# Performance work log

Measured on AMD Instinct MI355X. Metric: run time of the kernel, lower is better.

The kernel has to match this reference:

```python
import jax, jax.numpy as jnp
from jax import lax
import numpy as np

B, H, W, D_MODEL = 2, 64, 64, 192
D_INNER, D_STATE, DT_RANK = 384, 16, 12
L = H * W
LN_EPS = 1e-5


def setup_inputs() -> dict:
    ks = jax.random.split(jax.random.key(0), 12)
    rng = np.random.default_rng(0)
    perm = rng.permutation(L).astype(np.int32)

    def p(i, shape, scale=0.02):
        return jax.random.normal(ks[i], shape, dtype=jnp.float32) * scale

    return {
        "x": jax.random.normal(ks[0], (B, H, W, D_MODEL), dtype=jnp.float32),
        "condition": jax.random.normal(ks[1], (B, H, W, D_MODEL), dtype=jnp.float32),
        "W_in": p(2, (2 * D_INNER, D_MODEL)),
        "W_con": p(3, (D_INNER, D_MODEL)),
        "conv_w": p(4, (D_INNER, 1, 3, 3)),
        "conv_b": jnp.zeros((D_INNER,), jnp.float32),
        "con_conv_w": p(5, (D_INNER, 1, 3, 3)),
        "con_conv_b": jnp.zeros((D_INNER,), jnp.float32),
        "x_proj_w": p(6, (DT_RANK + 2 * D_STATE, D_INNER)),
        "dt_proj_w": p(7, (D_INNER, DT_RANK)),
        "dt_proj_b": p(8, (D_INNER,), 0.1),
        "A_logs": jnp.tile(jnp.log(jnp.arange(1, D_STATE + 1, dtype=jnp.float32))[None, :], (D_INNER, 1)),
        "Ds": jnp.ones((D_INNER,), jnp.float32),
        "ln_w": jnp.ones((D_INNER,), jnp.float32),
        "ln_b": jnp.zeros((D_INNER,), jnp.float32),
        "W_out": p(9, (D_MODEL, D_INNER)),
        "scan_path": jnp.asarray(perm),
        "rev_scan_path": jnp.asarray(np.argsort(perm).astype(np.int32)),
    }


def _dwconv(x, w, b):
    # depthwise 3x3 conv, SAME padding; x: [B, C, H, W], w: [C, 1, 3, 3]
    y = lax.conv_general_dilated(x, w, (1, 1), "SAME",
                                 dimension_numbers=("NCHW", "OIHW", "NCHW"),
                                 feature_group_count=x.shape[1])
    return y + b[None, :, None, None]


def _selective_scan(u, delta, A, Bs, Cs, D):
    # u, delta: [B, D, L]; A: [D, N]; Bs, Cs: [B, N, L]; D: [D]
    dA = jnp.exp(jnp.einsum("bdl,dn->lbdn", delta, A))          # [L, B, D, N]
    dBu = jnp.einsum("bdl,bnl,bdl->lbdn", delta, Bs, u)          # [L, B, D, N]
    Ct = jnp.transpose(Cs, (2, 0, 1))                             # [L, B, N]
    h0 = jnp.zeros(dA.shape[1:], dA.dtype)

    def step(h, inp):
        a, b, c = inp
        h = a * h + b
        return h, jnp.einsum("bdn,bn->bd", h, c)

    _, ys = lax.scan(step, h0, (dA, dBu, Ct))                     # ys: [L, B, D]
    y = jnp.transpose(ys, (1, 2, 0))                              # [B, D, L]
    return y + u * D[None, :, None]


def _forward(x, condition, W_in, W_con, conv_w, conv_b, con_conv_w, con_conv_b,
             x_proj_w, dt_proj_w, dt_proj_b, A_logs, Ds, ln_w, ln_b, W_out,
             scan_path, rev_scan_path):
    b, h, w, _ = x.shape
    l = h * w
    xz = x @ W_in.T                                               # [B, H, W, 2*Din]
    xa, z = jnp.split(xz, 2, axis=-1)
    z = jax.nn.silu(z)
    c = condition @ W_con.T
    xa = jax.nn.silu(_dwconv(jnp.transpose(xa, (0, 3, 1, 2)), conv_w, conv_b))
    c = jax.nn.silu(_dwconv(jnp.transpose(c, (0, 3, 1, 2)), con_conv_w, con_conv_b))
    d = xa.shape[1]
    xs = xa.reshape(b, d, l)[:, :, scan_path]                     # forward_permutation, K=1
    cs = c.reshape(b, d, l)[:, :, scan_path]
    x_dbl = jnp.einsum("bdl,cd->bcl", xs + cs, x_proj_w)          # [B, R+2N, L]
    r, n = dt_proj_w.shape[1], A_logs.shape[1]
    dts = jnp.einsum("brl,dr->bdl", x_dbl[:, :r], dt_proj_w)
    Bs = x_dbl[:, r:r + n]
    Cs = x_dbl[:, r + n:]
    A = -jnp.exp(A_logs)
    delta = jax.nn.softplus(dts + dt_proj_b[None, :, None])       # delta_softplus=True
    y = _selective_scan(xs, delta, A, Bs, Cs, Ds)                 # [B, D, L]
    y = y[:, :, rev_scan_path]                                    # backward_permutation
    y = jnp.transpose(y, (0, 2, 1))                               # [B, L, D]
    mu = jnp.mean(y, axis=-1, keepdims=True)
    var = jnp.var(y, axis=-1, keepdims=True)
    y = (y - mu) * lax.rsqrt(var + LN_EPS) * ln_w + ln_b          # out_norm
    y = y.reshape(b, h, w, d) * z
    return y @ W_out.T                                            # out_proj (no bias)


def reference(x, condition, W_in, W_con, conv_w, conv_b, con_conv_w, con_conv_b,
              x_proj_w, dt_proj_w, dt_proj_b, A_logs, Ds, ln_w, ln_b, W_out,
              scan_path, rev_scan_path):
    return _forward(x, condition, W_in, W_con, conv_w, conv_b, con_conv_w,
                    con_conv_b, x_proj_w, dt_proj_w, dt_proj_b, A_logs, Ds,
                    ln_w, ln_b, W_out, scan_path, rev_scan_path)
```

## Files before the change

### kernel.cpp

```cpp
#include <hip/hip_runtime.h>
#include <math.h>

#define BB 2
#define HH 64
#define WW 64
#define DM 192
#define DI 384
#define NS 16
#define DTR 12
#define LL 4096
#define ROWS (BB*LL)
#define NCHUNK 128
#define LCHUNK 32
#define NCOMBP 512
#define CSTRIDE ((size_t)BB * DI * 8)

typedef __attribute__((ext_vector_type(8))) short bf16x8;
typedef __attribute__((ext_vector_type(4))) float f32x4;

typedef __attribute__((address_space(3))) void        as3_void;
typedef __attribute__((address_space(1))) const void  as1_cvoid;

__device__ __forceinline__ void gl_lds16(const unsigned short* g, unsigned short* l) {
    __builtin_amdgcn_global_load_lds((as1_cvoid*)g, (as3_void*)l, 16, 0, 0);
}

__device__ __forceinline__ float silu_f(float v) {
    return v / (1.0f + __expf(-v));
}

__device__ __forceinline__ unsigned short f2bf(float f) {
    union { float f; unsigned int u; } c; c.f = f;
    unsigned int u = c.u;
    u += 0x7fffu + ((u >> 16) & 1u);
    return (unsigned short)(u >> 16);
}
__device__ __forceinline__ float bf2f(unsigned short h) {
    union { unsigned int u; float f; } c; c.u = ((unsigned int)h) << 16;
    return c.f;
}

__global__ __launch_bounds__(256) void prep_weights(
    const float* __restrict__ x, const float* __restrict__ cond,
    const float* __restrict__ w_in, const float* __restrict__ w_con,
    const float* __restrict__ w_out,
    const float* __restrict__ x_proj_w, const float* __restrict__ dt_w,
    unsigned short* __restrict__ w_in_bf, unsigned short* __restrict__ w_con_bf,
    unsigned short* __restrict__ w_out_bf, unsigned short* __restrict__ wc,
    unsigned short* __restrict__ x_bfo, unsigned short* __restrict__ c_bfo)
{
    int idx = blockIdx.x * 256 + threadIdx.x;
    if (idx < 73728) {
        const float4* src; ushort4* dst; int off;
        if (idx < 36864)      { src = (const float4*)w_in;  dst = (ushort4*)w_in_bf;  off = idx; }
        else if (idx < 55296) { src = (const float4*)w_con; dst = (ushort4*)w_con_bf; off = idx - 36864; }
        else                  { src = (const float4*)w_out; dst = (ushort4*)w_out_bf; off = idx - 55296; }
        float4 v = src[off];
        ushort4 o;
        o.x = f2bf(v.x); o.y = f2bf(v.y); o.z = f2bf(v.z); o.w = f2bf(v.w);
        dst[off] = o;
    } else if (idx < 73728 + NCOMBP * DI) {
        int e = idx - 73728;
        int row = e / DI, k = e - row * DI;
        float v = 0.f;
        if (row < 384) {
            const float* dw = dt_w + row * DTR;
            #pragma unroll
            for (int r = 0; r < DTR; ++r) v += dw[r] * x_proj_w[r * DI + k];
        } else if (row < 416) {
            v = x_proj_w[(12 + (row - 384)) * DI + k];
        }
        wc[e] = f2bf(v);
    } else if (idx < 73728 + NCOMBP * DI + 786432) {
        int e = idx - (73728 + NCOMBP * DI);
        const float4* src; ushort4* dst; int off;
        if (e < 393216) { src = (const float4*)x;    dst = (ushort4*)x_bfo; off = e; }
        else            { src = (const float4*)cond; dst = (ushort4*)c_bfo; off = e - 393216; }
        float4 v = src[off];
        ushort4 o;
        o.x = f2bf(v.x); o.y = f2bf(v.y); o.z = f2bf(v.z); o.w = f2bf(v.w);
        dst[off] = o;
    }
}

__global__ __launch_bounds__(256) void gemm_in(
    const unsigned short* __restrict__ x_bf, const unsigned short* __restrict__ cin_bf,
    const unsigned short* __restrict__ w_in_bf,
    const unsigned short* __restrict__ w_con_bf,
    unsigned short* __restrict__ xa_bf, unsigned short* __restrict__ z_bf,
    unsigned short* __restrict__ c_bf)
{
    const int zz = blockIdx.z;
    if (zz == 1 && blockIdx.y >= 3) return;
    const unsigned short* A = zz ? cin_bf : x_bf;
    const unsigned short* W = zz ? w_con_bf : w_in_bf;

    __shared__ __align__(16) unsigned short sA[128 * 32];
    __shared__ __align__(16) unsigned short sB[128 * 32];
    const int bm = blockIdx.x * 128;
    const int bn = blockIdx.y * 128;
    const int tid  = threadIdx.x;
    const int wave = tid >> 6;
    const int lane = tid & 63;
    const int quad = lane >> 4;
    const int l16  = lane & 15;
    const int srow = tid >> 2;
    const int scol = (tid & 3) * 8;

    f32x4 acc[2][8];
    #pragma unroll
    for (int rf = 0; rf < 2; ++rf)
        #pragma unroll
        for (int t = 0; t < 8; ++t) acc[rf][t] = (f32x4)(0.f);

    const unsigned short* gA0 = &A[(size_t)(bm + srow) * DM + scol];
    const unsigned short* gA1 = gA0 + (size_t)64 * DM;
    const unsigned short* gB0 = &W[(size_t)(bn + srow) * DM + scol];
    const unsigned short* gB1 = gB0 + (size_t)64 * DM;
    unsigned short* lA0 = &sA[wave * 512];
    unsigned short* lA1 = &sA[2048 + wave * 512];
    unsigned short* lB0 = &sB[wave * 512];
    unsigned short* lB1 = &sB[2048 + wave * 512];

    const int ar0 = (wave * 32 + l16) * 32 + quad * 8;
    const int ar1 = ar0 + 16 * 32;

    for (int k0 = 0; k0 < DM; k0 += 32) {
        gl_lds16(gA0 + k0, lA0);
        gl_lds16(gA1 + k0, lA1);
        gl_lds16(gB0 + k0, lB0);
        gl_lds16(gB1 + k0, lB1);
        __syncthreads();
        bf16x8 a0 = *(bf16x8*)&sA[ar0];
        bf16x8 a1 = *(bf16x8*)&sA[ar1];
        #pragma unroll
        for (int t = 0; t < 8; ++t) {
            bf16x8 b = *(bf16x8*)&sB[(t * 16 + l16) * 32 + quad * 8];
            acc[0][t] = __builtin_amdgcn_mfma_f32_16x16x32_bf16(a0, b, acc[0][t], 0, 0, 0);
            acc[1][t] = __builtin_amdgcn_mfma_f32_16x16x32_bf16(a1, b, acc[1][t], 0, 0, 0);
        }
        __syncthreads();
    }

    #pragma unroll
    for (int rf = 0; rf < 2; ++rf) {
        #pragma unroll
        for (int t = 0; t < 8; ++t) {
            int col = bn + t * 16 + l16;
            #pragma unroll
            for (int r = 0; r < 4; ++r) {
                int row = bm + wave * 32 + rf * 16 + quad * 4 + r;
                float v = acc[rf][t][r];
                if (zz == 0) {
                    if (col < 384) xa_bf[(size_t)row * 384 + col] = f2bf(v);
                    else           z_bf[(size_t)row * 384 + (col - 384)] = f2bf(silu_f(v));
                } else {
                    c_bf[(size_t)row * 384 + col] = f2bf(v);
                }
            }
        }
    }
}

__global__ __launch_bounds__(256) void gemm_comb(
    const unsigned short* __restrict__ A, const unsigned short* __restrict__ W,
    const float* __restrict__ bias, float* __restrict__ btct,
    unsigned short* __restrict__ du_lo)
{
    __shared__ __align__(16) unsigned short sA[128 * 32];
    __shared__ __align__(16) unsigned short sB[128 * 32];
    const int bm = blockIdx.x * 128;
    const int bn = blockIdx.y * 128;
    const int tid  = threadIdx.x;
    const int wave = tid >> 6;
    const int lane = tid & 63;
    const int quad = lane >> 4;
    const int l16  = lane & 15;
    const int srow = tid >> 2;
    const int scol = (tid & 3) * 8;

    f32x4 acc[2][8];
    #pragma unroll
    for (int rf = 0; rf < 2; ++rf)
        #pragma unroll
        for (int t = 0; t < 8; ++t) acc[rf][t] = (f32x4)(0.f);

    const unsigned short* gA0 = &A[(size_t)(bm + srow) * DI + scol];
    const unsigned short* gA1 = gA0 + (size_t)64 * DI;
    const unsigned short* gB0 = &W[(size_t)(bn + srow) * DI + scol];
    const unsigned short* gB1 = gB0 + (size_t)64 * DI;
    unsigned short* lA0 = &sA[wave * 512];
    unsigned short* lA1 = &sA[2048 + wave * 512];
    unsigned short* lB0 = &sB[wave * 512];
    unsigned short* lB1 = &sB[2048 + wave * 512];

    const int ar0 = (wave * 32 + l16) * 32 + quad * 8;
    const int ar1 = ar0 + 16 * 32;

    for (int k0 = 0; k0 < DI; k0 += 32) {
        gl_lds16(gA0 + k0, lA0);
        gl_lds16(gA1 + k0, lA1);
        gl_lds16(gB0 + k0, lB0);
        gl_lds16(gB1 + k0, lB1);
        __syncthreads();
        bf16x8 a0 = *(bf16x8*)&sA[ar0];
        bf16x8 a1 = *(bf16x8*)&sA[ar1];
        #pragma unroll
        for (int t = 0; t < 8; ++t) {
            bf16x8 b = *(bf16x8*)&sB[(t * 16 + l16) * 32 + quad * 8];
            acc[0][t] = __builtin_amdgcn_mfma_f32_16x16x32_bf16(a0, b, acc[0][t], 0, 0, 0);
            acc[1][t] = __builtin_amdgcn_mfma_f32_16x16x32_bf16(a1, b, acc[1][t], 0, 0, 0);
        }
        __syncthreads();
    }

    #pragma unroll
    for (int rf = 0; rf < 2; ++rf) {
        #pragma unroll
        for (int t = 0; t < 8; ++t) {
            int col = bn + t * 16 + l16;
            #pragma unroll
            for (int r = 0; r < 4; ++r) {
                int row = bm + wave * 32 + rf * 16 + quad * 4 + r;
                float v = acc[rf][t][r];
                if (col < 384) {
                    float a = v + bias[col];
                    float sp = (a > 20.f) ? a : log1pf(__expf(a));
                    du_lo[((size_t)row * 384 + col) * 2] = f2bf(sp);
                } else if (col < 416) {
                    int idx = col - 384;
                    int pos = (idx < 16) ? ((idx & 7) * 4 + (idx >> 3))
                                         : (((idx - 16) & 7) * 4 + 2 + ((idx - 16) >> 3));
                    btct[(size_t)row * 32 + pos] = v;
                }
            }
        }
    }
}

__global__ __launch_bounds__(256) void gemm_out_fused(
    const unsigned short* __restrict__ yt, const unsigned short* __restrict__ z,
    const int* __restrict__ rev_path,
    const float* __restrict__ ln_w, const float* __restrict__ ln_b,
    const unsigned short* __restrict__ W, float* __restrict__ out)
{
    __shared__ __align__(16) unsigned short sA[64 * 392];
    __shared__ __align__(16) unsigned short sB[64 * 32];
    const int bm = blockIdx.x * 64;
    const int bn = blockIdx.y * 64;
    const int tid = threadIdx.x;
    const int r   = tid >> 2;
    const int q4  = tid & 3;
    const int b   = bm >> 12;
    const int l   = (bm & (LL - 1)) + r;
    const int js  = rev_path[l];

    const unsigned short* yrow = yt + ((size_t)(b * LL + js)) * DI;
    const unsigned short* zrow = z  + ((size_t)(b * LL + l)) * DI;

    float s = 0.f, s2 = 0.f;
    #pragma unroll
    for (int i = 0; i < 12; ++i) {
        bf16x8 v = *(const bf16x8*)&yrow[i * 32 + q4 * 8];
        #pragma unroll
        for (int e = 0; e < 8; ++e) {
            float f = bf2f((unsigned short)v[e]);
            s += f; s2 += f * f;
        }
    }
    s  += __shfl_xor(s, 1);  s  += __shfl_xor(s, 2);
    s2 += __shfl_xor(s2, 1); s2 += __shfl_xor(s2, 2);
    const float mu  = s * (1.0f / DI);
    const float inv = rsqrtf(s2 * (1.0f / DI) - mu * mu + 1e-5f);

    #pragma unroll
    for (int i = 0; i < 12; ++i) {
        int c = i * 32 + q4 * 8;
        bf16x8 v  = *(const bf16x8*)&yrow[c];
        bf16x8 zv = *(const bf16x8*)&zrow[c];
        float4 wa = *(const float4*)&ln_w[c];
        float4 wb = *(const float4*)&ln_w[c + 4];
        float4 ba = *(const float4*)&ln_b[c];
        float4 bb = *(const float4*)&ln_b[c + 4];
        bf16x8 o;
        o[0] = (short)f2bf(((bf2f((unsigned short)v[0]) - mu) * inv * wa.x + ba.x) * bf2f((unsigned short)zv[0]));
        o[1] = (short)f2bf(((bf2f((unsigned short)v[1]) - mu) * inv * wa.y + ba.y) * bf2f((unsigned short)zv[1]));
        o[2] = (short)f2bf(((bf2f((unsigned short)v[2]) - mu) * inv * wa.z + ba.z) * bf2f((unsigned short)zv[2]));
        o[3] = (short)f2bf(((bf2f((unsigned short)v[3]) - mu) * inv * wa.w + ba.w) * bf2f((unsigned short)zv[3]));
        o[4] = (short)f2bf(((bf2f((unsigned short)v[4]) - mu) * inv * wb.x + bb.x) * bf2f((unsigned short)zv[4]));
        o[5] = (short)f2bf(((bf2f((unsigned short)v[5]) - mu) * inv * wb.y + bb.y) * bf2f((unsigned short)zv[5]));
        o[6] = (short)f2bf(((bf2f((unsigned short)v[6]) - mu) * inv * wb.z + bb.z) * bf2f((unsigned short)zv[6]));
        o[7] = (short)f2bf(((bf2f((unsigned short)v[7]) - mu) * inv * wb.w + bb.w) * bf2f((unsigned short)zv[7]));
        *(bf16x8*)&sA[r * 392 + c] = o;
    }

    const int wave = tid >> 6;
    const int lane = tid & 63;
    const int quad = lane >> 4;
    const int l16  = lane & 15;

    f32x4 acc[4];
    #pragma unroll
    for (int t = 0; t < 4; ++t) acc[t] = (f32x4)(0.f);

    const unsigned short* gB = &W[(size_t)(bn + r) * DI + q4 * 8];
    unsigned short* lB = &sB[wave * 512];
    const int abase = (wave * 16 + l16) * 392 + quad * 8;

    for (int k0 = 0; k0 < DI; k0 += 32) {
        gl_lds16(gB + k0, lB);
        __syncthreads();
        bf16x8 a = *(bf16x8*)&sA[abase + k0];
        #pragma unroll
        for (int t = 0; t < 4; ++t) {
            bf16x8 bfr = *(bf16x8*)&sB[(t * 16 + l16) * 32 + quad * 8];
            acc[t] = __builtin_amdgcn_mfma_f32_16x16x32_bf16(a, bfr, acc[t], 0, 0, 0);
        }
        __syncthreads();
    }

    #pragma unroll
    for (int t = 0; t < 4; ++t) {
        int col = bn + t * 16 + l16;
        #pragma unroll
        for (int rr = 0; rr < 4; ++rr) {
            int row = bm + wave * 16 + quad * 4 + rr;
            out[(size_t)row * DM + col] = acc[t][rr];
        }
    }
}

__global__ __launch_bounds__(256) void dwconv2_scatter(
    const unsigned short* __restrict__ xin, const unsigned short* __restrict__ cin,
    const float* __restrict__ wx, const float* __restrict__ bx,
    const float* __restrict__ wc, const float* __restrict__ bc,
    const int* __restrict__ rev_scan_path,
    unsigned short* __restrict__ du_hi,
    unsigned short* __restrict__ s_bf)
{
    const int tile = blockIdx.x;
    const int c0   = blockIdx.y * 32;
    const int b    = blockIdx.z;
    const int h0 = (tile >> 3) * 8, w0 = (tile & 7) * 8;
    __shared__ float smx[10 * 10 * 32];
    __shared__ float smc[10 * 10 * 32];
    __shared__ int   jtile[64];

    for (int idx = threadIdx.x; idx < 3200; idx += 256) {
        int pix = idx >> 5, ch = idx & 31;
        int py = pix / 10, px = pix - py * 10;
        int gh = h0 + py - 1, gw = w0 + px - 1;
        float vx = 0.f, vc = 0.f;
        if (gh >= 0 && gh < 64 && gw >= 0 && gw < 64) {
            size_t g = ((size_t)(b * LL + gh * 64 + gw)) * DI + c0 + ch;
            vx = bf2f(xin[g]); vc = bf2f(cin[g]);
        }
        smx[idx] = vx; smc[idx] = vc;
    }
    if (threadIdx.x < 64) {
        int l = (h0 + (threadIdx.x >> 3)) * 64 + (w0 + (threadIdx.x & 7));
        jtile[threadIdx.x] = rev_scan_path[l];
    }
    __syncthreads();

    const int ch = threadIdx.x & 31;
    const int pq = threadIdx.x >> 5;
    float wrx[9], wrc[9];
    #pragma unroll
    for (int k = 0; k < 9; ++k) {
        wrx[k] = wx[(c0 + ch) * 9 + k];
        wrc[k] = wc[(c0 + ch) * 9 + k];
    }
    const float bvx = bx[c0 + ch];
    const float bvc = bc[c0 + ch];

    #pragma unroll
    for (int i = 0; i < 8; ++i) {
        int p  = pq * 8 + i;
        int ph = p >> 3, pw = p & 7;
        float ax = bvx, ac = bvc;
        #pragma unroll
        for (int ki = 0; ki < 3; ++ki)
            #pragma unroll
            for (int kj = 0; kj < 3; ++kj) {
                int si = ((ph + ki) * 10 + (pw + kj)) * 32 + ch;
                ax += wrx[ki * 3 + kj] * smx[si];
                ac += wrc[ki * 3 + kj] * smc[si];
            }
        float xv = silu_f(ax);
        float sv = xv + silu_f(ac);
        size_t o = ((size_t)(b * LL + jtile[p])) * DI + c0 + ch;
        du_hi[o * 2 + 1] = f2bf(xv);
        s_bf[o]          = f2bf(sv);
    }
}

__global__ __launch_bounds__(256) void scan_chunkA(
    const unsigned int* __restrict__ du, const float* __restrict__ btct,
    const float* __restrict__ A_logs,
    float* __restrict__ chunkA, float* __restrict__ chunkB)
{
    const int c = blockIdx.x;
    const int g = blockIdx.y;
    const int b = blockIdx.z;
    const int t = threadIdx.x;
    const int grp = t >> 3, p = t & 7;
    const int d = g * 32 + grp;
    const float Av0 = -__expf(A_logs[d * NS + p]);
    const float Av1 = -__expf(A_logs[d * NS + p + 8]);
    const int j0 = c * LCHUNK;

    const unsigned int* dul = du + ((size_t)b * LL + j0) * DI + d;
    const float2*       bl  = (const float2*)btct + ((size_t)b * LL + j0) * 16 + p * 2;

    float h0 = 0.f, h1 = 0.f, Sd = 0.f;
    unsigned int duv[4]; float2 bv[4];
    #pragma unroll
    for (int q = 0; q < 4; ++q) {
        duv[q] = dul[(size_t)q * DI]; bv[q] = bl[(size_t)q * 16];
    }
    for (int j = 0; j < LCHUNK; j += 4) {
        unsigned int ndu[4]; float2 nb[4];
        if (j + 4 < LCHUNK) {
            #pragma unroll
            for (int q = 0; q < 4; ++q) {
                int jj = j + 4 + q;
                ndu[q] = dul[(size_t)jj * DI]; nb[q] = bl[(size_t)jj * 16];
            }
        }
        #pragma unroll
        for (int q = 0; q < 4; ++q) {
            float dv = bf2f((unsigned short)(duv[q] & 0xffff));
            float uv = bf2f((unsigned short)(duv[q] >> 16));
            float e0 = __expf(dv * Av0);
            float e1 = __expf(dv * Av1);
            float duu = dv * uv;
            h0 = e0 * h0 + bv[q].x * duu;
            h1 = e1 * h1 + bv[q].y * duu;
            Sd += dv;
        }
        #pragma unroll
        for (int q = 0; q < 4; ++q) { duv[q]=ndu[q]; bv[q]=nb[q]; }
    }
    size_t idx = (size_t)c * CSTRIDE + ((size_t)b * DI + d) * 8 + p;
    ((float2*)chunkA)[idx] = make_float2(__expf(Sd * Av0), __expf(Sd * Av1));
    ((float2*)chunkB)[idx] = make_float2(h0, h1);
}

__global__ __launch_bounds__(256) void scan_chunkC(
    const unsigned int* __restrict__ du, const float* __restrict__ btct,
    const float* __restrict__ A_logs, const float* __restrict__ Ds,
    const float* __restrict__ chunkA, const float* __restrict__ chunkB,
    unsigned short* __restrict__ yt)
{
    const int c = blockIdx.x;
    const int g = blockIdx.y;
    const int b = blockIdx.z;
    const int t = threadIdx.x;
    const int grp = t >> 3, p = t & 7;
    const int d = g * 32 + grp;
    const float Av0 = -__expf(A_logs[d * NS + p]);
    const float Av1 = -__expf(A_logs[d * NS + p + 8]);
    const float Dv = Ds[d];
    const int j0 = c * LCHUNK;

    const unsigned int* dul = du + ((size_t)b * LL + j0) * DI + d;
    const float4*       bcl = (const float4*)btct + ((size_t)b * LL + j0) * 8 + p;
    unsigned short* yl = yt + ((size_t)b * LL + j0) * DI + d;

    const size_t off = ((size_t)b * DI + d) * 8 + p;
    const float2* A2 = (const float2*)chunkA;
    const float2* B2 = (const float2*)chunkB;
    float h0 = 0.f, h1 = 0.f, P0 = 1.f, P1 = 1.f;
    for (int i = c - 1; i >= 0; --i) {
        size_t ix = (size_t)i * CSTRIDE + off;
        float2 a = A2[ix], bv = B2[ix];
        h0 += P0 * bv.x;  h1 += P1 * bv.y;
        P0 *= a.x;        P1 *= a.y;
        if (fmaxf(fabsf(P0), fabsf(P1)) < 1e-30f) break;
    }

    unsigned int duv[4]; float4 bc[4];
    #pragma unroll
    for (int q = 0; q < 4; ++q) {
        duv[q] = dul[(size_t)q * DI]; bc[q] = bcl[(size_t)q * 8];
    }
    for (int j = 0; j < LCHUNK; j += 4) {
        unsigned int ndu[4]; float4 nbc[4];
        if (j + 4 < LCHUNK) {
            #pragma unroll
            for (int q = 0; q < 4; ++q) {
                int jj = j + 4 + q;
                ndu[q] = dul[(size_t)jj * DI]; nbc[q] = bcl[(size_t)jj * 8];
            }
        }
        #pragma unroll
        for (int q = 0; q < 4; ++q) {
            float dv = bf2f((unsigned short)(duv[q] & 0xffff));
            float uv = bf2f((unsigned short)(duv[q] >> 16));
            float e0 = __expf(dv * Av0);
            float e1 = __expf(dv * Av1);
            float duu = dv * uv;
            h0 = e0 * h0 + bc[q].x * duu;
            h1 = e1 * h1 + bc[q].y * duu;
            float acc = h0 * bc[q].z + h1 * bc[q].w;
            acc += __shfl_xor(acc, 4, 8);
            acc += __shfl_xor(acc, 2, 8);
            acc += __shfl_xor(acc, 1, 8);
            if (p == 0) yl[(size_t)(j + q) * DI] = f2bf(acc + uv * Dv);
        }
        #pragma unroll
        for (int q = 0; q < 4; ++q) { duv[q]=ndu[q]; bc[q]=nbc[q]; }
    }
}

extern "C" void kernel_launch(void* const* d_in, const int* in_sizes, int n_in,
                              void* d_out, int out_size, void* d_ws, size_t ws_size,
                              hipStream_t stream) {
    const float* x          = (const float*)d_in[0];
    const float* cond       = (const float*)d_in[1];
    const float* W_in       = (const float*)d_in[2];
    const float* W_con      = (const float*)d_in[3];
    const float* conv_w     = (const float*)d_in[4];
    const float* conv_b     = (const float*)d_in[5];
    const float* con_conv_w = (const float*)d_in[6];
    const float* con_conv_b = (const float*)d_in[7];
    const float* x_proj_w   = (const float*)d_in[8];
    const float* dt_proj_w  = (const float*)d_in[9];
    const float* dt_proj_b  = (const float*)d_in[10];
    const float* A_logs     = (const float*)d_in[11];
    const float* Ds         = (const float*)d_in[12];
    const float* ln_w       = (const float*)d_in[13];
    const float* ln_b       = (const float*)d_in[14];
    const float* W_out      = (const float*)d_in[15];
    const int*   scan_path  = (const int*)d_in[16];
    const int*   rev_path   = (const int*)d_in[17];
    (void)scan_path;

    float* ws = (float*)d_ws;
    const size_t S  = (size_t)BB * LL * DI;
    const size_t SC = (size_t)NCHUNK * BB * DI * NS;
    float* ytslab  = ws + 0 * S;
    float* zslab   = ws + 1 * S;
    float* duslab  = ws + 2 * S;
    float* btct    = ws + 3 * S;
    float* chunkA  = btct + (size_t)BB * LL * 32;
    float* chunkB  = chunkA + SC;
    float* bfpool  = chunkB + SC;

    unsigned short* yt_bf    = (unsigned short*)ytslab;
    unsigned short* z_bf     = (unsigned short*)zslab;
    unsigned int*   du       = (unsigned int*)duslab;
    unsigned short* s_bf     = (unsigned short*)bfpool;
    unsigned short* xa_bf    = s_bf + (size_t)ROWS * DI;
    unsigned short* c_bf     = xa_bf + (size_t)ROWS * DI;
    unsigned short* w_in_bf  = c_bf + (size_t)ROWS * DI;
    unsigned short* w_con_bf = w_in_bf + 768 * DM;
    unsigned short* w_out_bf = w_con_bf + 384 * DM;
    unsigned short* wcomb_bf = w_out_bf + 192 * DI;
    unsigned short* x_bf2    = wcomb_bf + (size_t)NCOMBP * DI;
    unsigned short* cin_bf2  = x_bf2 + (size_t)ROWS * DM;

    prep_weights<<<4128, 256, 0, stream>>>(
        x, cond, W_in, W_con, W_out, x_proj_w, dt_proj_w,
        w_in_bf, w_con_bf, w_out_bf, wcomb_bf, x_bf2, cin_bf2);

    gemm_in<<<dim3(ROWS / 128, 6, 2), 256, 0, stream>>>(
        x_bf2, cin_bf2, w_in_bf, w_con_bf, xa_bf, z_bf, c_bf);
    dwconv2_scatter<<<dim3(64, 12, BB), 256, 0, stream>>>(
        xa_bf, c_bf, conv_w, conv_b, con_conv_w, con_conv_b,
        rev_path, (unsigned short*)du, s_bf);
    gemm_comb<<<dim3(ROWS / 128, NCOMBP / 128), 256, 0, stream>>>(
        s_bf, wcomb_bf, dt_proj_b, btct, (unsigned short*)du);
    scan_chunkA<<<dim3(NCHUNK, DI / 32, BB), 256, 0, stream>>>(
        du, btct, A_logs, chunkA, chunkB);
    scan_chunkC<<<dim3(NCHUNK, DI / 32, BB), 256, 0, stream>>>(
        du, btct, A_logs, Ds, chunkA, chunkB, yt_bf);
    gemm_out_fused<<<dim3(ROWS / 64, DM / 64), 256, 0, stream>>>(
        yt_bf, z_bf, rev_path, ln_w, ln_b, w_out_bf, (float*)d_out);
}
```

Baseline: 227.4 us.

## Double-buffer and swizzle LDS in GEMMs, shrink N tile, trim padded comb rows

All three bf16 MFMA GEMMs now double-buffer their LDS tiles, so the next K-slice's global-to-LDS load is issued while the current slice is multiplied, and one barrier per iteration is removed. The LDS layout gets an XOR swizzle on the 16-byte column groups to cut bank conflicts on fragment reads. gemm_in and gemm_comb use a 64-wide N tile instead of 128, which doubles the block count for occupancy. The padded combined-weight matrix shrinks from 512 to 448 rows, removing wasted MFMA work. The costs are more LDS per block, fewer accumulators per wave (less reuse of each A fragment), and more blocks re-reading A.

```diff
diff --git a/kernel.cpp b/kernel.cpp
--- a/kernel.cpp
+++ b/kernel.cpp
@@ -12,7 +12,7 @@
 #define ROWS (BB*LL)
 #define NCHUNK 128
 #define LCHUNK 32
-#define NCOMBP 512
+#define NCOMB 448
 #define CSTRIDE ((size_t)BB * DI * 8)
 
 typedef __attribute__((ext_vector_type(8))) short bf16x8;
@@ -59,7 +59,7 @@
         ushort4 o;
         o.x = f2bf(v.x); o.y = f2bf(v.y); o.z = f2bf(v.z); o.w = f2bf(v.w);
         dst[off] = o;
-    } else if (idx < 73728 + NCOMBP * DI) {
+    } else if (idx < 73728 + NCOMB * DI) {
         int e = idx - 73728;
         int row = e / DI, k = e - row * DI;
         float v = 0.f;
@@ -71,8 +71,8 @@
             v = x_proj_w[(12 + (row - 384)) * DI + k];
         }
         wc[e] = f2bf(v);
-    } else if (idx < 73728 + NCOMBP * DI + 786432) {
-        int e = idx - (73728 + NCOMBP * DI);
+    } else if (idx < 73728 + NCOMB * DI + 786432) {
+        int e = idx - (73728 + NCOMB * DI);
         const float4* src; ushort4* dst; int off;
         if (e < 393216) { src = (const float4*)x;    dst = (ushort4*)x_bfo; off = e; }
         else            { src = (const float4*)cond; dst = (ushort4*)c_bfo; off = e - 393216; }
@@ -91,61 +91,67 @@
     unsigned short* __restrict__ c_bf)
 {
     const int zz = blockIdx.z;
-    if (zz == 1 && blockIdx.y >= 3) return;
+    if (zz == 1 && blockIdx.y >= 6) return;
     const unsigned short* A = zz ? cin_bf : x_bf;
     const unsigned short* W = zz ? w_con_bf : w_in_bf;
 
-    __shared__ __align__(16) unsigned short sA[128 * 32];
-    __shared__ __align__(16) unsigned short sB[128 * 32];
+    __shared__ __align__(16) unsigned short sA[2 * 128 * 32];
+    __shared__ __align__(16) unsigned short sB[2 * 64 * 32];
     const int bm = blockIdx.x * 128;
-    const int bn = blockIdx.y * 128;
+    const int bn = blockIdx.y * 64;
     const int tid  = threadIdx.x;
     const int wave = tid >> 6;
     const int lane = tid & 63;
     const int quad = lane >> 4;
     const int l16  = lane & 15;
     const int srow = tid >> 2;
-    const int scol = (tid & 3) * 8;
-
-    f32x4 acc[2][8];
+    const int scol = ((tid & 3) ^ ((tid >> 3) & 3)) * 8;
+    const int rswz = (quad ^ ((l16 >> 1) & 3)) * 8;
+
+    f32x4 acc[2][4];
     #pragma unroll
     for (int rf = 0; rf < 2; ++rf)
         #pragma unroll
-        for (int t = 0; t < 8; ++t) acc[rf][t] = (f32x4)(0.f);
+        for (int t = 0; t < 4; ++t) acc[rf][t] = (f32x4)(0.f);
 
     const unsigned short* gA0 = &A[(size_t)(bm + srow) * DM + scol];
     const unsigned short* gA1 = gA0 + (size_t)64 * DM;
-    const unsigned short* gB0 = &W[(size_t)(bn + srow) * DM + scol];
-    const unsigned short* gB1 = gB0 + (size_t)64 * DM;
-    unsigned short* lA0 = &sA[wave * 512];
-    unsigned short* lA1 = &sA[2048 + wave * 512];
-    unsigned short* lB0 = &sB[wave * 512];
-    unsigned short* lB1 = &sB[2048 + wave * 512];
-
-    const int ar0 = (wave * 32 + l16) * 32 + quad * 8;
+    const unsigned short* gB  = &W[(size_t)(bn + srow) * DM + scol];
+
+    gl_lds16(gA0, &sA[wave * 512]);
+    gl_lds16(gA1, &sA[2048 + wave * 512]);
+    gl_lds16(gB,  &sB[wave * 512]);
+    __syncthreads();
+
+    const int ar0 = (wave * 32 + l16) * 32 + rswz;
     const int ar1 = ar0 + 16 * 32;
 
-    for (int k0 = 0; k0 < DM; k0 += 32) {
-        gl_lds16(gA0 + k0, lA0);
-        gl_lds16(gA1 + k0, lA1);
-        gl_lds16(gB0 + k0, lB0);
-        gl_lds16(gB1 + k0, lB1);
+    for (int t = 0; t < 6; ++t) {
+        const int cur = t & 1;
+        if (t + 1 < 6) {
+            const int k = (t + 1) * 32;
+            const int nb = cur ^ 1;
+            gl_lds16(gA0 + k, &sA[nb * 4096 + wave * 512]);
+            gl_lds16(gA1 + k, &sA[nb * 4096 + 2048 + wave * 512]);
+            gl_lds16(gB  + k, &sB[nb * 2048 + wave * 512]);
+        }
+        const unsigned short* cA = &sA[cur * 4096];
+        const unsigned short* cB = &sB[cur * 2048];
+        bf16x8 a0 = *(bf16x8*)&cA[ar0];
+        bf16x8 a1 = *(bf16x8*)&cA[ar1];
+        #pragma unroll
+        for (int n = 0; n < 4; ++n) {
+            bf16x8 b = *(bf16x8*)&cB[(n * 16 + l16) * 32 + rswz];
+            acc[0][n] = __builtin_amdgcn_mfma_f32_16x16x32_bf16(a0, b, acc[0][n], 0, 0, 0);
+            acc[1][n] = __builtin_amdgcn_mfma_f32_16x16x32_bf16(a1, b, acc[1][n], 0, 0, 0);
+        }
         __syncthreads();
-        bf16x8 a0 = *(bf16x8*)&sA[ar0];
-        bf16x8 a1 = *(bf16x8*)&sA[ar1];
-        #pragma unroll
-        for (int t = 0; t < 8; ++t) {
-            bf16x8 b = *(bf16x8*)&sB[(t * 16 + l16) * 32 + quad * 8];
-            acc[0][t] = __builtin_amdgcn_mfma_f32_16x16x32_bf16(a0, b, acc[0][t], 0, 0, 0);
-            acc[1][t] = __builtin_amdgcn_mfma_f32_16x16x32_bf16(a1, b, acc[1][t], 0, 0, 0);
-        }
-        __syncthreads();
     }
 
     #pragma unroll
     for (int rf = 0; rf < 2; ++rf) {
         #pragma unroll
-        for (int t = 0; t < 8; ++t) {
+        for (int t = 0; t < 4; ++t) {
             int col = bn + t * 16 + l16;
             #pragma unroll
             for (int r = 0; r < 4; ++r) {
@@ -167,57 +173,63 @@
     const float* __restrict__ bias, float* __restrict__ btct,
     unsigned short* __restrict__ du_lo)
 {
-    __shared__ __align__(16) unsigned short sA[128 * 32];
-    __shared__ __align__(16) unsigned short sB[128 * 32];
+    __shared__ __align__(16) unsigned short sA[2 * 128 * 32];
+    __shared__ __align__(16) unsigned short sB[2 * 64 * 32];
     const int bm = blockIdx.x * 128;
-    const int bn = blockIdx.y * 128;
+    const int bn = blockIdx.y * 64;
     const int tid  = threadIdx.x;
     const int wave = tid >> 6;
     const int lane = tid & 63;
     const int quad = lane >> 4;
     const int l16  = lane & 15;
     const int srow = tid >> 2;
-    const int scol = (tid & 3) * 8;
-
-    f32x4 acc[2][8];
+    const int scol = ((tid & 3) ^ ((tid >> 3) & 3)) * 8;
+    const int rswz = (quad ^ ((l16 >> 1) & 3)) * 8;
+
+    f32x4 acc[2][4];
     #pragma unroll
     for (int rf = 0; rf < 2; ++rf)
         #pragma unroll
-        for (int t = 0; t < 8; ++t) acc[rf][t] = (f32x4)(0.f);
+        for (int t = 0; t < 4; ++t) acc[rf][t] = (f32x4)(0.f);
 
     const unsigned short* gA0 = &A[(size_t)(bm + srow) * DI + scol];
     const unsigned short* gA1 = gA0 + (size_t)64 * DI;
-    const unsigned short* gB0 = &W[(size_t)(bn + srow) * DI + scol];
-    const unsigned short* gB1 = gB0 + (size_t)64 * DI;
-    unsigned short* lA0 = &sA[wave * 512];
-    unsigned short* lA1 = &sA[2048 + wave * 512];
-    unsigned short* lB0 = &sB[wave * 512];
-    unsigned short* lB1 = &sB[2048 + wave * 512];
-
-    const int ar0 = (wave * 32 + l16) * 32 + quad * 8;
+    const unsigned short* gB  = &W[(size_t)(bn + srow) * DI + scol];
+
+    gl_lds16(gA0, &sA[wave * 512]);
+    gl_lds16(gA1, &sA[2048 + wave * 512]);
+    gl_lds16(gB,  &sB[wave * 512]);
+    __syncthreads();
+
+    const int ar0 = (wave * 32 + l16) * 32 + rswz;
     const int ar1 = ar0 + 16 * 32;
 
-    for (int k0 = 0; k0 < DI; k0 += 32) {
-        gl_lds16(gA0 + k0, lA0);
-        gl_lds16(gA1 + k0, lA1);
-        gl_lds16(gB0 + k0, lB0);
-        gl_lds16(gB1 + k0, lB1);
+    for (int t = 0; t < 12; ++t) {
+        const int cur = t & 1;
+        if (t + 1 < 12) {
+            const int k = (t + 1) * 32;
+            const int nb = cur ^ 1;
+            gl_lds16(gA0 + k, &sA[nb * 4096 + wave * 512]);
+            gl_lds16(gA1 + k, &sA[nb * 4096 + 2048 + wave * 512]);
+            gl_lds16(gB  + k, &sB[nb * 2048 + wave * 512]);
+        }
+        const unsigned short* cA = &sA[cur * 4096];
+        const unsigned short* cB = &sB[cur * 2048];
+        bf16x8 a0 = *(bf16x8*)&cA[ar0];
+        bf16x8 a1 = *(bf16x8*)&cA[ar1];
+        #pragma unroll
+        for (int n = 0; n < 4; ++n) {
+            bf16x8 b = *(bf16x8*)&cB[(n * 16 + l16) * 32 + rswz];
+            acc[0][n] = __builtin_amdgcn_mfma_f32_16x16x32_bf16(a0, b, acc[0][n], 0, 0, 0);
+            acc[1][n] = __builtin_amdgcn_mfma_f32_16x16x32_bf16(a1, b, acc[1][n], 0, 0, 0);
+        }
         __syncthreads();
-        bf16x8 a0 = *(bf16x8*)&sA[ar0];
-        bf16x8 a1 = *(bf16x8*)&sA[ar1];
-        #pragma unroll
-        for (int t = 0; t < 8; ++t) {
-            bf16x8 b = *(bf16x8*)&sB[(t * 16 + l16) * 32 + quad * 8];
-            acc[0][t] = __builtin_amdgcn_mfma_f32_16x16x32_bf16(a0, b, acc[0][t], 0, 0, 0);
-            acc[1][t] = __builtin_amdgcn_mfma_f32_16x16x32_bf16(a1, b, acc[1][t], 0, 0, 0);
-        }
-        __syncthreads();
     }
 
     #pragma unroll
     for (int rf = 0; rf < 2; ++rf) {
         #pragma unroll
-        for (int t = 0; t < 8; ++t) {
+        for (int t = 0; t < 4; ++t) {
             int col = bn + t * 16 + l16;
             #pragma unroll
             for (int r = 0; r < 4; ++r) {
@@ -245,7 +257,7 @@
     const unsigned short* __restrict__ W, float* __restrict__ out)
 {
     __shared__ __align__(16) unsigned short sA[64 * 392];
-    __shared__ __align__(16) unsigned short sB[64 * 32];
+    __shared__ __align__(16) unsigned short sB[2 * 64 * 32];
     const int bm = blockIdx.x * 64;
     const int bn = blockIdx.y * 64;
     const int tid = threadIdx.x;
@@ -298,23 +310,29 @@
     const int lane = tid & 63;
     const int quad = lane >> 4;
     const int l16  = lane & 15;
+    const int scol = ((tid & 3) ^ ((tid >> 3) & 3)) * 8;
+    const int rswz = (quad ^ ((l16 >> 1) & 3)) * 8;
 
     f32x4 acc[4];
     #pragma unroll
     for (int t = 0; t < 4; ++t) acc[t] = (f32x4)(0.f);
 
-    const unsigned short* gB = &W[(size_t)(bn + r) * DI + q4 * 8];
-    unsigned short* lB = &sB[wave * 512];
+    const unsigned short* gB = &W[(size_t)(bn + r) * DI + scol];
     const int abase = (wave * 16 + l16) * 392 + quad * 8;
 
-    for (int k0 = 0; k0 < DI; k0 += 32) {
-        gl_lds16(gB + k0, lB);
-        __syncthreads();
-        bf16x8 a = *(bf16x8*)&sA[abase + k0];
-        #pragma unroll
-        for (int t = 0; t < 4; ++t) {
-            bf16x8 bfr = *(bf16x8*)&sB[(t * 16 + l16) * 32 + quad * 8];
-            acc[t] = __builtin_amdgcn_mfma_f32_16x16x32_bf16(a, bfr, acc[t], 0, 0, 0);
+    gl_lds16(gB, &sB[wave * 512]);
+    __syncthreads();
+
+    for (int t = 0; t < 12; ++t) {
+        const int cur = t & 1;
+        if (t + 1 < 12)
+            gl_lds16(gB + (t + 1) * 32, &sB[(cur ^ 1) * 2048 + wave * 512]);
+        bf16x8 a = *(bf16x8*)&sA[abase + t * 32];
+        const unsigned short* cB = &sB[cur * 2048];
+        #pragma unroll
+        for (int n = 0; n < 4; ++n) {
+            bf16x8 bfr = *(bf16x8*)&cB[(n * 16 + l16) * 32 + rswz];
+            acc[n] = __builtin_amdgcn_mfma_f32_16x16x32_bf16(a, bfr, acc[n], 0, 0, 0);
         }
         __syncthreads();
     }
@@ -558,19 +576,19 @@
     unsigned short* w_con_bf = w_in_bf + 768 * DM;
     unsigned short* w_out_bf = w_con_bf + 384 * DM;
     unsigned short* wcomb_bf = w_out_bf + 192 * DI;
-    unsigned short* x_bf2    = wcomb_bf + (size_t)NCOMBP * DI;
+    unsigned short* x_bf2    = wcomb_bf + (size_t)NCOMB * DI;
     unsigned short* cin_bf2  = x_bf2 + (size_t)ROWS * DM;
 
-    prep_weights<<<4128, 256, 0, stream>>>(
+    prep_weights<<<4032, 256, 0, stream>>>(
         x, cond, W_in, W_con, W_out, x_proj_w, dt_proj_w,
         w_in_bf, w_con_bf, w_out_bf, wcomb_bf, x_bf2, cin_bf2);
 
-    gemm_in<<<dim3(ROWS / 128, 6, 2), 256, 0, stream>>>(
+    gemm_in<<<dim3(ROWS / 128, 12, 2), 256, 0, stream>>>(
         x_bf2, cin_bf2, w_in_bf, w_con_bf, xa_bf, z_bf, c_bf);
     dwconv2_scatter<<<dim3(64, 12, BB), 256, 0, stream>>>(
         xa_bf, c_bf, conv_w, conv_b, con_conv_w, con_conv_b,
         rev_path, (unsigned short*)du, s_bf);
-    gemm_comb<<<dim3(ROWS / 128, NCOMBP / 128), 256, 0, stream>>>(
+    gemm_comb<<<dim3(ROWS / 128, NCOMB / 64), 256, 0, stream>>>(
         s_bf, wcomb_bf, dt_proj_b, btct, (unsigned short*)du);
     scan_chunkA<<<dim3(NCHUNK, DI / 32, BB), 256, 0, stream>>>(
         du, btct, A_logs, chunkA, chunkB);
```

Result: faster. 202.9 us (-10.8%).
